# Kernel optimization log

Measured on AMD Instinct MI355X. Metric: run time of the kernel, lower is better.

## Reference

```python
import jax, jax.numpy as jnp
import numpy as np

EPS = 1e-5

def _ln(x, g, b):
    mu = jnp.mean(x, axis=-1, keepdims=True)
    var = jnp.var(x, axis=-1, keepdims=True)
    return (x - mu) * jax.lax.rsqrt(var + EPS) * g + b

def setup_inputs() -> dict:
    key = jax.random.key(0)
    ks = jax.random.split(key, 8)
    B, S, D, DK, DV = 8, 2048, 1024, 128, 128
    sD = 1.0 / np.sqrt(D)
    sDV = 1.0 / np.sqrt(DV)
    sH = 1.0 / np.sqrt(4 * D)
    return {
        "x": jax.random.normal(ks[0], (B, S, D), jnp.float32),
        "ln1_g": jnp.ones((D,), jnp.float32),
        "ln1_b": jnp.zeros((D,), jnp.float32),
        "Wq": jax.random.normal(ks[1], (D, DK), jnp.float32) * sD,
        "bq": jnp.zeros((DK,), jnp.float32),
        "Wk": jax.random.normal(ks[2], (D, DK), jnp.float32) * sD,
        "bk": jnp.zeros((DK,), jnp.float32),
        "Wv": jax.random.normal(ks[3], (D, DV), jnp.float32) * sD,
        "bv": jnp.zeros((DV,), jnp.float32),
        "Wo": jax.random.normal(ks[4], (DV, D), jnp.float32) * sDV,
        "bo": jnp.zeros((D,), jnp.float32),
        "ln2_g": jnp.ones((D,), jnp.float32),
        "ln2_b": jnp.zeros((D,), jnp.float32),
        "W1": jax.random.normal(ks[5], (D, 4 * D), jnp.float32) * sD,
        "b1": jnp.zeros((4 * D,), jnp.float32),
        "W2": jax.random.normal(ks[6], (4 * D, D), jnp.float32) * sH,
        "b2": jnp.zeros((D,), jnp.float32),
    }

def reference(x, ln1_g, ln1_b, Wq, bq, Wk, bk, Wv, bv, Wo, bo, ln2_g, ln2_b, W1, b1, W2, b2):
    # Block.forward (scaling_test=None): pre-LN, naive full attention, residual MLP
    xn = _ln(x, ln1_g, ln1_b)                       # [B,S,D]
    q = xn @ Wq + bq                                # [B,S,DK]
    k = xn @ Wk + bk                                # [B,S,DK]
    v = xn @ Wv + bv                                # [B,S,DV]
    scale = 1.0 / np.sqrt(q.shape[-1])
    S = jnp.einsum("bqd,bkd->bqk", q, k) * scale    # [B,S,S] materialized scores
    A = jax.nn.softmax(S, axis=-1)
    H = jnp.einsum("bqk,bkv->bqv", A, v)            # [B,S,DV]
    y = xn + (H @ Wo + bo)                          # note: residual uses ln1(x), as in source
    h = _ln(y, ln2_g, ln2_b)
    mlp = jax.nn.gelu(h @ W1 + b1, approximate=False) @ W2 + b2
    return y + mlp
```

## Files before the change

kernel.cpp:

```cpp
#include <hip/hip_runtime.h>
#include <math.h>

#define M_TOT   16384
#define D_MODEL 1024
#define D_HEAD  128
#define SEQ     2048
#define NBATCH  8
#define D_FF    4096

typedef _Float16 f16x8 __attribute__((ext_vector_type(8)));
typedef _Float16 f16x4 __attribute__((ext_vector_type(4)));
typedef float    f32x4 __attribute__((ext_vector_type(4)));

#define ATT_SCALE 0.08838834764831845f

__device__ __forceinline__ void gload_lds16(const _Float16* g, _Float16* l) {
  __builtin_amdgcn_global_load_lds(
      (const __attribute__((address_space(1))) unsigned int*)g,
      (__attribute__((address_space(3))) unsigned int*)l, 16, 0, 0);
}
__device__ __forceinline__ unsigned short f16bits(float v) {
  union { _Float16 f; unsigned short u; } cv; cv.f = (_Float16)v; return cv.u;
}
__device__ __forceinline__ float gelu_f(float x) {
  const float t = 0.7978845608028654f * x * (1.0f + 0.044715f * x * x);
  const float e = __expf(2.0f * t);
  const float th = 1.0f - 2.0f / (e + 1.0f);
  return 0.5f * x * (1.0f + th);
}
__device__ __forceinline__ void bar_sync() {
  __asm__ volatile("" ::: "memory");
  __builtin_amdgcn_s_barrier();
  __asm__ volatile("" ::: "memory");
}
__device__ __forceinline__ int swzb(int row, int quad) {
  const int e = (((row & 1) << 2) | quad) ^ ((row >> 1) & 7);
  return ((row >> 1) << 7) | (e << 4);
}
__device__ __forceinline__ void ds_read128o(f16x8& d, unsigned addr, int imm) {
  asm volatile("ds_read_b128 %0, %1 offset:%2" : "=v"(d) : "v"(addr), "i"(imm));
}

__global__ __launch_bounds__(256) void convt_kernel(const float* __restrict__ in,
                                                    _Float16* __restrict__ out,
                                                    int K, int N) {
  __shared__ float t[32][33];
  const int n0 = blockIdx.x * 32, k0 = blockIdx.y * 32;
  const int tx = threadIdx.x & 31, ty = threadIdx.x >> 5;
#pragma unroll
  for (int r = 0; r < 4; r++)
    t[ty + 8 * r][tx] = in[(size_t)(k0 + ty + 8 * r) * N + n0 + tx];
  __syncthreads();
#pragma unroll
  for (int r = 0; r < 4; r++)
    out[(size_t)(n0 + ty + 8 * r) * K + k0 + tx] = (_Float16)t[tx][ty + 8 * r];
}

template <bool WF32>
__global__ __launch_bounds__(256) void ln_kernel(const float* __restrict__ in,
                                                 const float* __restrict__ gamma,
                                                 const float* __restrict__ beta,
                                                 float* __restrict__ of,
                                                 _Float16* __restrict__ oh) {
  __shared__ float shs[4], shq[4];
  const int row = blockIdx.x;
  const int t = threadIdx.x;
  float4 v = ((const float4*)(in + (size_t)row * D_MODEL))[t];
  float s = v.x + v.y + v.z + v.w;
  float q = v.x * v.x + v.y * v.y + v.z * v.z + v.w * v.w;
#pragma unroll
  for (int o = 32; o > 0; o >>= 1) {
    s += __shfl_down(s, o, 64);
    q += __shfl_down(q, o, 64);
  }
  const int lane = t & 63, w = t >> 6;
  if (lane == 0) { shs[w] = s; shq[w] = q; }
  __syncthreads();
  if (t == 0) {
    shs[0] = shs[0] + shs[1] + shs[2] + shs[3];
    shq[0] = shq[0] + shq[1] + shq[2] + shq[3];
  }
  __syncthreads();
  const float mu = shs[0] * (1.0f / D_MODEL);
  const float var = shq[0] * (1.0f / D_MODEL) - mu * mu;
  const float rs = rsqrtf(var + 1e-5f);
  float4 gv = ((const float4*)gamma)[t];
  float4 bv = ((const float4*)beta)[t];
  float4 o;
  o.x = (v.x - mu) * rs * gv.x + bv.x;
  o.y = (v.y - mu) * rs * gv.y + bv.y;
  o.z = (v.z - mu) * rs * gv.z + bv.z;
  o.w = (v.w - mu) * rs * gv.w + bv.w;
  if (WF32) ((float4*)(of + (size_t)row * D_MODEL))[t] = o;
  f16x4 h4 = {(_Float16)o.x, (_Float16)o.y, (_Float16)o.z, (_Float16)o.w};
  ((f16x4*)(oh + (size_t)row * D_MODEL))[t] = h4;
}


struct Frag { f16x8 a[8]; f16x8 b[4]; };

__device__ __forceinline__ void rd_frags(Frag& f, unsigned bA, unsigned bB) {
#pragma unroll
  for (int m = 0; m < 8; ++m) ds_read128o(f.a[m], bA, m * 1024);
#pragma unroll
  for (int n = 0; n < 4; ++n) ds_read128o(f.b[n], bB, n * 1024);
}
__device__ __forceinline__ void mfma32(f32x4 acc[8][4], const Frag& f) {
#pragma unroll
  for (int m = 0; m < 8; ++m)
#pragma unroll
    for (int n = 0; n < 4; ++n)
      acc[m][n] = __builtin_amdgcn_mfma_f32_16x16x32_f16(f.a[m], f.b[n], acc[m][n], 0, 0, 0);
}

#define STAGE_A(JT)                                                       \
  {                                                                       \
    _Float16* ps_ = SM + (((JT) & 3) * 16384) + ldsA;                     \
    const size_t kp_ = (size_t)(JT) * 32;                                 \
    gload_lds16(Ag0 + kp_, ps_);                                          \
    gload_lds16(Ag0 + 16 * (size_t)K + kp_, ps_ + 512);                   \
  }
#define STAGE_B(JT)                                                       \
  {                                                                       \
    _Float16* ps_ = SM + (((JT) & 3) * 16384) + ldsB;                     \
    const size_t kp_ = (size_t)(JT) * 32;                                 \
    gload_lds16(Bg0 + kp_, ps_);                                          \
    gload_lds16(Bg0 + 16 * (size_t)K + kp_, ps_ + 512);                   \
  }

#define KITER(CUR, NXT, JT, RD, PF, WVM)                                       \
  {                                                                            \
    asm volatile("s_waitcnt lgkmcnt(0)" ::: "memory");                         \
    __builtin_amdgcn_sched_barrier(0);                                         \
    bar_sync();                                                                \
    if (RD) {                                                                  \
      const unsigned sb_ = ((unsigned)(((JT) + 1) & 3)) << 15;                 \
      rd_frags(NXT, fbaseA + sb_, fbaseB + sb_);                               \
    }                                                                          \
    if (PF) { STAGE_A((JT) + 3); STAGE_B((JT) + 3); }                          \
    __builtin_amdgcn_sched_barrier(0);                                         \
    __builtin_amdgcn_s_setprio(1);                                             \
    mfma32(acc, CUR);                                                          \
    __builtin_amdgcn_s_setprio(0);                                             \
    if ((WVM) == 4) { asm volatile("s_waitcnt vmcnt(4)" ::: "memory"); bar_sync(); } \
    if ((WVM) == 0) { asm volatile("s_waitcnt vmcnt(0)" ::: "memory"); bar_sync(); } \
  }

template <int MODE>
__global__ __launch_bounds__(512, 2) void mfma_gemm256(
    const _Float16* __restrict__ A, const _Float16* __restrict__ BT,
    const float* __restrict__ bias, const float* __restrict__ res,
    void* __restrict__ Cout, int M, int N, int K) {
  __shared__ __attribute__((aligned(16))) _Float16 SM[4 * 16384];
  const int tid = threadIdx.x;
  const int lane = tid & 63, w = tid >> 6;
  const int l15 = lane & 15, quad = lane >> 4;
  const int wm = w >> 2, wn = w & 3;

  const int nwg = gridDim.x;
  const int bid = (blockIdx.x & 7) * (nwg >> 3) + (blockIdx.x >> 3);
  const int nbx = N >> 8;
  const int bx = bid % nbx, by = bid / nbx;
  const int row0 = by << 8, col0 = bx << 8;

  const int rp = lane >> 3;
  const int el = (lane & 7) ^ rp;
  const int lr = (rp << 1) | (el >> 2);
  const int lc = (el & 3) << 3;
  const _Float16* Ag0 = A + (size_t)(row0 + w * 32 + lr) * K + lc;
  const _Float16* Bg0 = BT + (size_t)(col0 + w * 32 + lr) * K + lc;
  const int ldsA = w * 1024;
  const int ldsB = 8192 + w * 1024;

  const unsigned lds0 =
      (unsigned)(size_t)(__attribute__((address_space(3))) _Float16*)&SM[0];
  const unsigned esw = (unsigned)((((l15 & 1) << 2) | quad) ^ ((l15 >> 1) & 7));
  const unsigned rl128 = (unsigned)(l15 >> 1) << 7;
  const unsigned fbaseA = lds0 + (unsigned)(wm * 8192) + rl128 + (esw << 4);
  const unsigned fbaseB = lds0 + 16384u + (unsigned)(wn * 4096) + rl128 + (esw << 4);

  const f32x4 zero = {0.f, 0.f, 0.f, 0.f};
  f32x4 acc[8][4];
#pragma unroll
  for (int m = 0; m < 8; ++m)
#pragma unroll
    for (int n = 0; n < 4; ++n) acc[m][n] = zero;

  const int NKT = K >> 5;
  Frag fA, fB;

  for (int t = 0; t < 3; ++t) { STAGE_A(t); STAGE_B(t); }
  asm volatile("s_waitcnt vmcnt(4)" ::: "memory");
  bar_sync();
  rd_frags(fA, fbaseA, fbaseB);

  int j = 0;
#pragma unroll 1
  for (; j + 5 < NKT; j += 2) {
    KITER(fA, fB, j,     1, 1, 4);
    KITER(fB, fA, j + 1, 1, 1, 4);
  }
  KITER(fA, fB, NKT - 4, 1, 1, 4);
  KITER(fB, fA, NKT - 3, 1, 0, 0);
  KITER(fA, fB, NKT - 2, 1, 0, -1);
  KITER(fB, fA, NKT - 1, 0, 0, -1);

  const int colb = col0 + wn * 64 + l15;
  if (MODE == 0) {
    float* C = (float*)Cout;
    float bv[4];
#pragma unroll
    for (int n = 0; n < 4; ++n) bv[n] = bias[colb + n * 16];
#pragma unroll
    for (int m = 0; m < 8; ++m)
#pragma unroll
      for (int r = 0; r < 4; ++r) {
        const int row = row0 + wm * 128 + m * 16 + quad * 4 + r;
        const size_t base = (size_t)row * N + colb;
        const float* rp2 = res + base;
        float* cp = C + base;
#pragma unroll
        for (int n = 0; n < 4; ++n) cp[n * 16] = acc[m][n][r] + bv[n] + rp2[n * 16];
      }
  } else {
    _Float16* C = (_Float16*)Cout;
    float bv[4];
#pragma unroll
    for (int n = 0; n < 4; ++n) bv[n] = bias[colb + n * 16];
#pragma unroll
    for (int m = 0; m < 8; ++m)
#pragma unroll
      for (int r = 0; r < 4; ++r) {
        const int row = row0 + wm * 128 + m * 16 + quad * 4 + r;
        _Float16* cp = C + (size_t)row * N + colb;
#pragma unroll
        for (int n = 0; n < 4; ++n) cp[n * 16] = (_Float16)gelu_f(acc[m][n][r] + bv[n]);
      }
  }
  (void)M;
}

template <int MODE>
__global__ __launch_bounds__(256) void mfma_gemm(const _Float16* __restrict__ A,
                                                 const _Float16* __restrict__ BT,
                                                 const float* __restrict__ b0p,
                                                 const float* __restrict__ b1p,
                                                 const float* __restrict__ b2p,
                                                 const float* __restrict__ res,
                                                 void* __restrict__ Cout,
                                                 _Float16* __restrict__ vtout,
                                                 int M, int N, int K) {
  __shared__ _Float16 SMEM[2 * 128 * 32];
  _Float16* As = SMEM;
  _Float16* Bs = SMEM + 128 * 32;
  const int tid = threadIdx.x;
  const int lane = tid & 63, w = tid >> 6;
  const int wr = w >> 1, wc = w & 1;
  const int row0 = blockIdx.y << 7, col0 = blockIdx.x << 7;
  const int l15 = lane & 15, quad = lane >> 4;
  const f32x4 zero = {0.f, 0.f, 0.f, 0.f};
  f32x4 acc[4][4];
#pragma unroll
  for (int i = 0; i < 4; i++)
#pragma unroll
    for (int j = 0; j < 4; j++) acc[i][j] = zero;

  const int srow = lane >> 2;
  const int scol = (lane & 3) << 3;
  const _Float16* Ag = A + (size_t)(row0 + w * 32 + srow) * K + scol;
  const _Float16* Bg = BT + (size_t)(col0 + w * 32 + srow) * K + scol;

  for (int k0 = 0; k0 < K; k0 += 32) {
#pragma unroll
    for (int p = 0; p < 2; p++) {
      gload_lds16(Ag + (size_t)(p * 16) * K + k0, &As[(w * 32 + p * 16) * 32]);
      gload_lds16(Bg + (size_t)(p * 16) * K + k0, &Bs[(w * 32 + p * 16) * 32]);
    }
    __syncthreads();
    f16x8 af[4], bfr[4];
#pragma unroll
    for (int i = 0; i < 4; i++) {
      af[i]  = *(const f16x8*)&As[(wr * 64 + i * 16 + l15) * 32 + quad * 8];
      bfr[i] = *(const f16x8*)&Bs[(wc * 64 + i * 16 + l15) * 32 + quad * 8];
    }
#pragma unroll
    for (int i = 0; i < 4; i++)
#pragma unroll
      for (int j = 0; j < 4; j++)
        acc[i][j] = __builtin_amdgcn_mfma_f32_16x16x32_f16(af[i], bfr[j], acc[i][j], 0, 0, 0);
    __syncthreads();
  }

  if (MODE == 0) {
    float* C = (float*)Cout;
    float bv4[4];
#pragma unroll
    for (int j = 0; j < 4; j++) bv4[j] = b0p[col0 + wc * 64 + j * 16 + l15];
#pragma unroll
    for (int i = 0; i < 4; i++)
#pragma unroll
      for (int r = 0; r < 4; r++) {
        const int row = row0 + wr * 64 + i * 16 + quad * 4 + r;
        const size_t base = (size_t)row * N + col0 + wc * 64 + l15;
        const float* rp = res + base;
        float* cp = C + base;
#pragma unroll
        for (int j = 0; j < 4; j++)
          cp[j * 16] = acc[i][j][r] + bv4[j] + rp[j * 16];
      }
  } else if (MODE == 1) {
    _Float16* C = (_Float16*)Cout;
    float bv4[4];
#pragma unroll
    for (int j = 0; j < 4; j++) bv4[j] = b0p[col0 + wc * 64 + j * 16 + l15];
#pragma unroll
    for (int i = 0; i < 4; i++)
#pragma unroll
      for (int r = 0; r < 4; r++) {
        const int row = row0 + wr * 64 + i * 16 + quad * 4 + r;
        _Float16* cp = C + (size_t)row * N + col0 + wc * 64 + l15;
#pragma unroll
        for (int j = 0; j < 4; j++)
          cp[j * 16] = (_Float16)gelu_f(acc[i][j][r] + bv4[j]);
      }
  } else {
    _Float16* qkout = (_Float16*)Cout;
    const int bx = blockIdx.x;
    if (bx < 2) {
      const float* bp = (bx == 0) ? b0p : b1p;
      const float sc = (bx == 0) ? ATT_SCALE : 1.0f;
      const int cofs = bx * 128 + wc * 64 + l15;
      float bv4[4];
#pragma unroll
      for (int j = 0; j < 4; j++) bv4[j] = bp[wc * 64 + j * 16 + l15];
#pragma unroll
      for (int i = 0; i < 4; i++)
#pragma unroll
        for (int r = 0; r < 4; r++) {
          const int row = row0 + wr * 64 + i * 16 + quad * 4 + r;
          _Float16* cp = qkout + (size_t)row * 256 + cofs;
#pragma unroll
          for (int j = 0; j < 4; j++)
            cp[j * 16] = (_Float16)((acc[i][j][r] + bv4[j]) * sc);
        }
    } else {
      _Float16* Ts = SMEM;
      float bv4[4];
#pragma unroll
      for (int j = 0; j < 4; j++) bv4[j] = b2p[wc * 64 + j * 16 + l15];
      const int bb = row0 >> 11, s0 = row0 & 2047;
#pragma unroll
      for (int c = 0; c < 4; c++) {
        __syncthreads();
        if (wr == (c >> 1)) {
#pragma unroll
          for (int ii = 0; ii < 2; ii++) {
            const int i = (c & 1) * 2 + ii;
#pragma unroll
            for (int j = 0; j < 4; j++) {
              const int vd = wc * 64 + j * 16 + l15;
              const int slocal = ii * 16 + quad * 4;
              ushort4 h;
              h.x = f16bits(acc[i][j][0] + bv4[j]);
              h.y = f16bits(acc[i][j][1] + bv4[j]);
              h.z = f16bits(acc[i][j][2] + bv4[j]);
              h.w = f16bits(acc[i][j][3] + bv4[j]);
              *(ushort4*)&Ts[vd * 40 + slocal] = h;
            }
          }
        }
        __syncthreads();
#pragma unroll
        for (int p = 0; p < 2; p++) {
          const int idx = tid + p * 256;
          const int vd = idx >> 2, s8 = (idx & 3) * 8;
          uint4 d = *(const uint4*)&Ts[vd * 40 + s8];
          *(uint4*)&vtout[((size_t)bb * 128 + vd) * SEQ + s0 + c * 32 + s8] = d;
        }
      }
    }
  }
}

__global__ __launch_bounds__(256) void flash_attn_mfma(const _Float16* __restrict__ qk,
                                                       const _Float16* __restrict__ vt,
                                                       _Float16* __restrict__ H) {
  __shared__ _Float16 Ks[2][64][136];
  __shared__ _Float16 Vs[128][72];
  __shared__ _Float16 Ps[4][16][72];
  const int b = blockIdx.y, q0 = blockIdx.x * 64;
  const int tid = threadIdx.x;
  const int lane = tid & 63, w = tid >> 6;
  const int l15 = lane & 15, quad = lane >> 4;

  f16x8 qf[4];
  {
    const _Float16* qrow = qk + ((size_t)(b * SEQ + q0 + w * 16 + l15)) * 256 + quad * 8;
#pragma unroll
    for (int ks = 0; ks < 4; ks++) qf[ks] = *(const f16x8*)(qrow + ks * 32);
  }
  const f32x4 zero = {0.f, 0.f, 0.f, 0.f};
  f32x4 O[8];
#pragma unroll
  for (int i = 0; i < 8; i++) O[i] = zero;
  float m_r[4] = {-1e30f, -1e30f, -1e30f, -1e30f};
  float l_r[4] = {0.f, 0.f, 0.f, 0.f};

  const _Float16* kg0 = qk + (size_t)(b * SEQ) * 256 + 128 + (size_t)(tid >> 4) * 256 + (tid & 15) * 8;
  const _Float16* vg0 = vt + (size_t)b * 128 * SEQ + (size_t)((tid >> 3)) * SEQ + (tid & 7) * 8;
  uint4 kp[4], vp[4];

#define LOAD_TILE(kt)                                                            \
  {                                                                              \
    const _Float16* kg = kg0 + (size_t)(kt) * 64 * 256;                          \
    const _Float16* vg = vg0 + (size_t)(kt) * 64;                                \
    _Pragma("unroll") for (int p = 0; p < 4; p++) {                              \
      kp[p] = *(const uint4*)(kg + (size_t)p * 16 * 256);                        \
      vp[p] = *(const uint4*)(vg + (size_t)p * 32 * SEQ);                        \
    }                                                                            \
  }
#define STORE_K(buf)                                                             \
  _Pragma("unroll") for (int p = 0; p < 4; p++)                                  \
      *(uint4*)&Ks[buf][(tid >> 4) + 16 * p][(tid & 15) * 8] = kp[p];
#define STORE_V()                                                                \
  _Pragma("unroll") for (int p = 0; p < 4; p++)                                  \
      *(uint4*)&Vs[(tid >> 3) + 32 * p][(tid & 7) * 8] = vp[p];

  LOAD_TILE(0);
  STORE_K(0);
  STORE_V();
  __syncthreads();

  const int NT = SEQ / 64;
  for (int kt = 0; kt < NT; kt++) {
    const int cur = kt & 1;
    if (kt + 1 < NT) LOAD_TILE(kt + 1);

    f32x4 s4[4];
#pragma unroll
    for (int nt = 0; nt < 4; nt++) {
      s4[nt] = zero;
#pragma unroll
      for (int ks = 0; ks < 4; ks++) {
        f16x8 kf = *(const f16x8*)&Ks[cur][nt * 16 + l15][ks * 32 + quad * 8];
        s4[nt] = __builtin_amdgcn_mfma_f32_16x16x32_f16(qf[ks], kf, s4[nt], 0, 0, 0);
      }
    }
    float rmax[4], alpha[4], rsum[4];
#pragma unroll
    for (int r = 0; r < 4; r++)
      rmax[r] = fmaxf(fmaxf(s4[0][r], s4[1][r]), fmaxf(s4[2][r], s4[3][r]));
#pragma unroll
    for (int o = 1; o < 16; o <<= 1)
#pragma unroll
      for (int r = 0; r < 4; r++) rmax[r] = fmaxf(rmax[r], __shfl_xor(rmax[r], o, 64));
#pragma unroll
    for (int r = 0; r < 4; r++) {
      const float nm = fmaxf(m_r[r], rmax[r]);
      alpha[r] = __expf(m_r[r] - nm);
      m_r[r] = nm;
#pragma unroll
      for (int nt = 0; nt < 4; nt++) s4[nt][r] = __expf(s4[nt][r] - nm);
      rsum[r] = s4[0][r] + s4[1][r] + s4[2][r] + s4[3][r];
    }
#pragma unroll
    for (int o = 1; o < 16; o <<= 1)
#pragma unroll
      for (int r = 0; r < 4; r++) rsum[r] += __shfl_xor(rsum[r], o, 64);
#pragma unroll
    for (int r = 0; r < 4; r++) {
      l_r[r] = l_r[r] * alpha[r] + rsum[r];
#pragma unroll
      for (int i = 0; i < 8; i++) O[i][r] *= alpha[r];
    }
#pragma unroll
    for (int nt = 0; nt < 4; nt++)
#pragma unroll
      for (int r = 0; r < 4; r++)
        Ps[w][quad * 4 + r][nt * 16 + l15] = (_Float16)s4[nt][r];
    f16x8 pa[2];
#pragma unroll
    for (int ks = 0; ks < 2; ks++)
      pa[ks] = *(const f16x8*)&Ps[w][l15][ks * 32 + quad * 8];
#pragma unroll
    for (int ks = 0; ks < 2; ks++)
#pragma unroll
      for (int vt8 = 0; vt8 < 8; vt8++) {
        f16x8 vf = *(const f16x8*)&Vs[vt8 * 16 + l15][ks * 32 + quad * 8];
        O[vt8] = __builtin_amdgcn_mfma_f32_16x16x32_f16(pa[ks], vf, O[vt8], 0, 0, 0);
      }

    if (kt + 1 < NT) {
      STORE_K(cur ^ 1);
      __syncthreads();
      STORE_V();
      __syncthreads();
    }
  }
#pragma unroll
  for (int r = 0; r < 4; r++) {
    const float inv = 1.0f / l_r[r];
    _Float16* hp = H + (size_t)(b * SEQ + q0 + w * 16 + quad * 4 + r) * D_HEAD;
#pragma unroll
    for (int vt8 = 0; vt8 < 8; vt8++)
      hp[vt8 * 16 + l15] = (_Float16)(O[vt8][r] * inv);
  }
}

extern "C" void kernel_launch(void* const* d_in, const int* in_sizes, int n_in,
                              void* d_out, int out_size, void* d_ws, size_t ws_size,
                              hipStream_t stream) {
  const float* x     = (const float*)d_in[0];
  const float* ln1_g = (const float*)d_in[1];
  const float* ln1_b = (const float*)d_in[2];
  const float* Wq    = (const float*)d_in[3];
  const float* bq    = (const float*)d_in[4];
  const float* Wk    = (const float*)d_in[5];
  const float* bk    = (const float*)d_in[6];
  const float* Wv    = (const float*)d_in[7];
  const float* bv    = (const float*)d_in[8];
  const float* Wo    = (const float*)d_in[9];
  const float* bo    = (const float*)d_in[10];
  const float* ln2_g = (const float*)d_in[11];
  const float* ln2_b = (const float*)d_in[12];
  const float* W1    = (const float*)d_in[13];
  const float* b1    = (const float*)d_in[14];
  const float* W2    = (const float*)d_in[15];
  const float* b2    = (const float*)d_in[16];
  float* out = (float*)d_out;

  char* ws = (char*)d_ws;
  const size_t MB = 1024 * 1024;
  _Float16* W1T   = (_Float16*)(ws);
  _Float16* W2T   = (_Float16*)(ws + 8 * MB);
  _Float16* WqkvT = (_Float16*)(ws + 16 * MB);
  _Float16* WoT   = (_Float16*)(ws + 16 * MB + 768 * 1024);
  float*    xn_f32 = (float*)(ws + 20 * MB);
  _Float16* xn_f16 = (_Float16*)(ws + 84 * MB);
  _Float16* qkb  = (_Float16*)(ws + 116 * MB);
  _Float16* vtb  = (_Float16*)(ws + 124 * MB);
  _Float16* Hb   = (_Float16*)(ws + 128 * MB);
  _Float16* act  = (_Float16*)(ws + 20 * MB);
  _Float16* h16  = (_Float16*)(ws + 148 * MB);

  convt_kernel<<<dim3(D_FF / 32, D_MODEL / 32), 256, 0, stream>>>(W1, W1T, D_MODEL, D_FF);
  convt_kernel<<<dim3(D_MODEL / 32, D_FF / 32), 256, 0, stream>>>(W2, W2T, D_FF, D_MODEL);
  convt_kernel<<<dim3(D_HEAD / 32, D_MODEL / 32), 256, 0, stream>>>(Wq, WqkvT, D_MODEL, D_HEAD);
  convt_kernel<<<dim3(D_HEAD / 32, D_MODEL / 32), 256, 0, stream>>>(Wk, WqkvT + 128 * 1024, D_MODEL, D_HEAD);
  convt_kernel<<<dim3(D_HEAD / 32, D_MODEL / 32), 256, 0, stream>>>(Wv, WqkvT + 256 * 1024, D_MODEL, D_HEAD);
  convt_kernel<<<dim3(D_MODEL / 32, D_HEAD / 32), 256, 0, stream>>>(Wo, WoT, D_HEAD, D_MODEL);
  ln_kernel<true><<<dim3(M_TOT), 256, 0, stream>>>(x, ln1_g, ln1_b, xn_f32, xn_f16);
  mfma_gemm<2><<<dim3(3, M_TOT / 128), 256, 0, stream>>>(
      xn_f16, WqkvT, bq, bk, bv, nullptr, qkb, vtb, M_TOT, 384, D_MODEL);
  flash_attn_mfma<<<dim3(SEQ / 64, NBATCH), 256, 0, stream>>>(qkb, vtb, Hb);
  mfma_gemm256<0><<<dim3((D_MODEL / 256) * (M_TOT / 256)), 512, 0, stream>>>(
      Hb, WoT, bo, xn_f32, out, M_TOT, D_MODEL, D_HEAD);
  ln_kernel<false><<<dim3(M_TOT), 256, 0, stream>>>(out, ln2_g, ln2_b, nullptr, h16);
  mfma_gemm256<1><<<dim3((D_FF / 256) * (M_TOT / 256)), 512, 0, stream>>>(
      h16, W1T, b1, nullptr, act, M_TOT, D_FF, D_MODEL);
  mfma_gemm256<0><<<dim3((D_MODEL / 256) * (M_TOT / 256)), 512, 0, stream>>>(
      act, W2T, b2, out, out, M_TOT, D_MODEL, D_FF);

  (void)in_sizes; (void)n_in; (void)out_size; (void)ws_size;
}
```

Baseline: 646.5 us.

## Restructure GEMM main loop into four-phase interleaved LDS-read/MFMA/prefetch schedule

Replaces the double-buffered register fragment scheme (read all next-tile fragments while computing the current tile) with a four-phase per-K-tile schedule. Each phase reads a subset of A/B fragments, issues one global-to-LDS prefetch, then runs eight MFMAs, separated by barriers. This cuts register pressure from holding two full fragment sets and spreads global loads across the iteration, but it adds many more barriers per K step and exposes LDS read latency inside each iteration, since there is no cross-iteration fragment prefetch.

```diff
diff --git a/kernel.cpp b/kernel.cpp
--- a/kernel.cpp
+++ b/kernel.cpp
@@ -33,13 +33,10 @@
   __builtin_amdgcn_s_barrier();
   __asm__ volatile("" ::: "memory");
 }
-__device__ __forceinline__ int swzb(int row, int quad) {
-  const int e = (((row & 1) << 2) | quad) ^ ((row >> 1) & 7);
-  return ((row >> 1) << 7) | (e << 4);
-}
 __device__ __forceinline__ void ds_read128o(f16x8& d, unsigned addr, int imm) {
   asm volatile("ds_read_b128 %0, %1 offset:%2" : "=v"(d) : "v"(addr), "i"(imm));
 }
+#define MFMA16(a, b, c) __builtin_amdgcn_mfma_f32_16x16x32_f16((a), (b), (c), 0, 0, 0)
 
 __global__ __launch_bounds__(256) void convt_kernel(const float* __restrict__ in,
                                                     _Float16* __restrict__ out,
@@ -97,51 +94,69 @@
 }
 
 
-struct Frag { f16x8 a[8]; f16x8 b[4]; };
-
-__device__ __forceinline__ void rd_frags(Frag& f, unsigned bA, unsigned bB) {
-#pragma unroll
-  for (int m = 0; m < 8; ++m) ds_read128o(f.a[m], bA, m * 1024);
-#pragma unroll
-  for (int n = 0; n < 4; ++n) ds_read128o(f.b[n], bB, n * 1024);
-}
-__device__ __forceinline__ void mfma32(f32x4 acc[8][4], const Frag& f) {
-#pragma unroll
-  for (int m = 0; m < 8; ++m)
-#pragma unroll
-    for (int n = 0; n < 4; ++n)
-      acc[m][n] = __builtin_amdgcn_mfma_f32_16x16x32_f16(f.a[m], f.b[n], acc[m][n], 0, 0, 0);
-}
-
-#define STAGE_A(JT)                                                       \
-  {                                                                       \
-    _Float16* ps_ = SM + (((JT) & 3) * 16384) + ldsA;                     \
-    const size_t kp_ = (size_t)(JT) * 32;                                 \
-    gload_lds16(Ag0 + kp_, ps_);                                          \
-    gload_lds16(Ag0 + 16 * (size_t)K + kp_, ps_ + 512);                   \
-  }
-#define STAGE_B(JT)                                                       \
-  {                                                                       \
-    _Float16* ps_ = SM + (((JT) & 3) * 16384) + ldsB;                     \
-    const size_t kp_ = (size_t)(JT) * 32;                                 \
-    gload_lds16(Bg0 + kp_, ps_);                                          \
-    gload_lds16(Bg0 + 16 * (size_t)K + kp_, ps_ + 512);                   \
-  }
-
-#define KITER(CUR, NXT, JT, RD, PF, WVM)                                       \
-  {                                                                            \
-    asm volatile("s_waitcnt lgkmcnt(0)" ::: "memory");                         \
-    __builtin_amdgcn_sched_barrier(0);                                         \
-    bar_sync();                                                                \
-    if (RD) {                                                                  \
-      const unsigned sb_ = ((unsigned)(((JT) + 1) & 3)) << 15;                 \
-      rd_frags(NXT, fbaseA + sb_, fbaseB + sb_);                               \
-    }                                                                          \
-    if (PF) { STAGE_A((JT) + 3); STAGE_B((JT) + 3); }                          \
-    __builtin_amdgcn_sched_barrier(0);                                         \
-    __builtin_amdgcn_s_setprio(1);                                             \
-    mfma32(acc, CUR);                                                          \
-    __builtin_amdgcn_s_setprio(0);                                             \
+#define STG_A1(JT) gload_lds16(Ag0 + (size_t)(JT) * 32, SM + (((JT) & 3) * 16384) + ldsA)
+#define STG_A2(JT) gload_lds16(Ag0 + 16 * (size_t)K + (size_t)(JT) * 32, SM + (((JT) & 3) * 16384) + ldsA + 512)
+#define STG_B1(JT) gload_lds16(Bg0 + (size_t)(JT) * 32, SM + (((JT) & 3) * 16384) + ldsB)
+#define STG_B2(JT) gload_lds16(Bg0 + 16 * (size_t)K + (size_t)(JT) * 32, SM + (((JT) & 3) * 16384) + ldsB + 512)
+
+#define KITER4(JT, PF, WVM)                                                         \
+  {                                                                                 \
+    const unsigned sb_ = ((unsigned)((JT) & 3)) << 15;                              \
+    const unsigned bA_ = fbaseA + sb_;                                              \
+    const unsigned bB_ = fbaseB + sb_;                                              \
+    f16x8 fa0, fa1, fa2, fa3, fa4, fa5, fa6, fa7, fb0, fb1, fb2, fb3;               \
+                  \
+    ds_read128o(fa0, bA_, 0);    ds_read128o(fa1, bA_, 1024);                       \
+    ds_read128o(fa2, bA_, 2048); ds_read128o(fa3, bA_, 3072);                       \
+    ds_read128o(fb0, bB_, 0);    ds_read128o(fb1, bB_, 1024);                       \
+    if (PF) { STG_A1((JT) + 3); }                                                   \
+    bar_sync();                                                                     \
+    asm volatile("s_waitcnt lgkmcnt(0)" ::: "memory");                              \
+    __builtin_amdgcn_sched_barrier(0);                                              \
+    __builtin_amdgcn_s_setprio(1);                                                  \
+    acc[0][0] = MFMA16(fa0, fb0, acc[0][0]); acc[0][1] = MFMA16(fa0, fb1, acc[0][1]); \
+    acc[1][0] = MFMA16(fa1, fb0, acc[1][0]); acc[1][1] = MFMA16(fa1, fb1, acc[1][1]); \
+    acc[2][0] = MFMA16(fa2, fb0, acc[2][0]); acc[2][1] = MFMA16(fa2, fb1, acc[2][1]); \
+    acc[3][0] = MFMA16(fa3, fb0, acc[3][0]); acc[3][1] = MFMA16(fa3, fb1, acc[3][1]); \
+    __builtin_amdgcn_s_setprio(0);                                                  \
+    bar_sync();                                                                     \
+                       \
+    ds_read128o(fb2, bB_, 2048); ds_read128o(fb3, bB_, 3072);                       \
+    if (PF) { STG_A2((JT) + 3); }                                                   \
+    bar_sync();                                                                     \
+    asm volatile("s_waitcnt lgkmcnt(0)" ::: "memory");                              \
+    __builtin_amdgcn_sched_barrier(0);                                              \
+    __builtin_amdgcn_s_setprio(1);                                                  \
+    acc[0][2] = MFMA16(fa0, fb2, acc[0][2]); acc[0][3] = MFMA16(fa0, fb3, acc[0][3]); \
+    acc[1][2] = MFMA16(fa1, fb2, acc[1][2]); acc[1][3] = MFMA16(fa1, fb3, acc[1][3]); \
+    acc[2][2] = MFMA16(fa2, fb2, acc[2][2]); acc[2][3] = MFMA16(fa2, fb3, acc[2][3]); \
+    acc[3][2] = MFMA16(fa3, fb2, acc[3][2]); acc[3][3] = MFMA16(fa3, fb3, acc[3][3]); \
+    __builtin_amdgcn_s_setprio(0);                                                  \
+    bar_sync();                                                                     \
+                       \
+    ds_read128o(fa4, bA_, 4096); ds_read128o(fa5, bA_, 5120);                       \
+    ds_read128o(fa6, bA_, 6144); ds_read128o(fa7, bA_, 7168);                       \
+    if (PF) { STG_B1((JT) + 3); }                                                   \
+    bar_sync();                                                                     \
+    asm volatile("s_waitcnt lgkmcnt(0)" ::: "memory");                              \
+    __builtin_amdgcn_sched_barrier(0);                                              \
+    __builtin_amdgcn_s_setprio(1);                                                  \
+    acc[4][0] = MFMA16(fa4, fb0, acc[4][0]); acc[4][1] = MFMA16(fa4, fb1, acc[4][1]); \
+    acc[5][0] = MFMA16(fa5, fb0, acc[5][0]); acc[5][1] = MFMA16(fa5, fb1, acc[5][1]); \
+    acc[6][0] = MFMA16(fa6, fb0, acc[6][0]); acc[6][1] = MFMA16(fa6, fb1, acc[6][1]); \
+    acc[7][0] = MFMA16(fa7, fb0, acc[7][0]); acc[7][1] = MFMA16(fa7, fb1, acc[7][1]); \
+    __builtin_amdgcn_s_setprio(0);                                                  \
+    bar_sync();                                                                     \
+         \
+    if (PF) { STG_B2((JT) + 3); }                                                   \
+    bar_sync();                                                                     \
+    __builtin_amdgcn_s_setprio(1);                                                  \
+    acc[4][2] = MFMA16(fa4, fb2, acc[4][2]); acc[4][3] = MFMA16(fa4, fb3, acc[4][3]); \
+    acc[5][2] = MFMA16(fa5, fb2, acc[5][2]); acc[5][3] = MFMA16(fa5, fb3, acc[5][3]); \
+    acc[6][2] = MFMA16(fa6, fb2, acc[6][2]); acc[6][3] = MFMA16(fa6, fb3, acc[6][3]); \
+    acc[7][2] = MFMA16(fa7, fb2, acc[7][2]); acc[7][3] = MFMA16(fa7, fb3, acc[7][3]); \
+    __builtin_amdgcn_s_setprio(0);                                                  \
+    if ((WVM) == 8) { asm volatile("s_waitcnt vmcnt(8)" ::: "memory"); bar_sync(); } \
     if ((WVM) == 4) { asm volatile("s_waitcnt vmcnt(4)" ::: "memory"); bar_sync(); } \
     if ((WVM) == 0) { asm volatile("s_waitcnt vmcnt(0)" ::: "memory"); bar_sync(); } \
   }
@@ -187,23 +202,17 @@
     for (int n = 0; n < 4; ++n) acc[m][n] = zero;
 
   const int NKT = K >> 5;
-  Frag fA, fB;
-
-  for (int t = 0; t < 3; ++t) { STAGE_A(t); STAGE_B(t); }
-  asm volatile("s_waitcnt vmcnt(4)" ::: "memory");
+
+  for (int t = 0; t < 3; ++t) { STG_A1(t); STG_A2(t); STG_B1(t); STG_B2(t); }
+  asm volatile("s_waitcnt vmcnt(8)" ::: "memory");
   bar_sync();
-  rd_frags(fA, fbaseA, fbaseB);
 
   int j = 0;
 #pragma unroll 1
-  for (; j + 5 < NKT; j += 2) {
-    KITER(fA, fB, j,     1, 1, 4);
-    KITER(fB, fA, j + 1, 1, 1, 4);
-  }
-  KITER(fA, fB, NKT - 4, 1, 1, 4);
-  KITER(fB, fA, NKT - 3, 1, 0, 0);
-  KITER(fA, fB, NKT - 2, 1, 0, -1);
-  KITER(fB, fA, NKT - 1, 0, 0, -1);
+  for (; j + 3 < NKT; ++j) { KITER4(j, 1, 8); }
+  KITER4(NKT - 3, 0, 4);
+  KITER4(NKT - 2, 0, 0);
+  KITER4(NKT - 1, 0, -1);
 
   const int colb = col0 + wn * 64 + l15;
   if (MODE == 0) {
```

Result: no change. 649.7 us (+0.5%).

## Restructure GEMM main loop to 64-wide K tiles with 8-phase interleaved staging

Applied to the files above, without the earlier changes.

Changes the 256x256 f16 MFMA GEMM main loop from 32-wide K tiles with quad buffering to 64-wide K tiles with double buffering. Each K tile is split into four sub-phases, and A/B loads for future tiles are interleaved between MFMA sub-blocks. The LDS layout and swizzle are rewritten to 128-byte rows. The goal is fewer barriers per unit of work and better overlap of global-to-LDS loads with MFMA, at the cost of more barriers per iteration and a more intricate, less flexible schedule.

```diff
diff --git a/kernel.cpp b/kernel.cpp
--- a/kernel.cpp
+++ b/kernel.cpp
@@ -33,13 +33,10 @@
   __builtin_amdgcn_s_barrier();
   __asm__ volatile("" ::: "memory");
 }
-__device__ __forceinline__ int swzb(int row, int quad) {
-  const int e = (((row & 1) << 2) | quad) ^ ((row >> 1) & 7);
-  return ((row >> 1) << 7) | (e << 4);
-}
 __device__ __forceinline__ void ds_read128o(f16x8& d, unsigned addr, int imm) {
   asm volatile("ds_read_b128 %0, %1 offset:%2" : "=v"(d) : "v"(addr), "i"(imm));
 }
+#define MFMA16(a, b, c) __builtin_amdgcn_mfma_f32_16x16x32_f16((a), (b), (c), 0, 0, 0)
 
 __global__ __launch_bounds__(256) void convt_kernel(const float* __restrict__ in,
                                                     _Float16* __restrict__ out,
@@ -97,53 +94,73 @@
 }
 
 
-struct Frag { f16x8 a[8]; f16x8 b[4]; };
-
-__device__ __forceinline__ void rd_frags(Frag& f, unsigned bA, unsigned bB) {
-#pragma unroll
-  for (int m = 0; m < 8; ++m) ds_read128o(f.a[m], bA, m * 1024);
-#pragma unroll
-  for (int n = 0; n < 4; ++n) ds_read128o(f.b[n], bB, n * 1024);
-}
-__device__ __forceinline__ void mfma32(f32x4 acc[8][4], const Frag& f) {
-#pragma unroll
-  for (int m = 0; m < 8; ++m)
-#pragma unroll
-    for (int n = 0; n < 4; ++n)
-      acc[m][n] = __builtin_amdgcn_mfma_f32_16x16x32_f16(f.a[m], f.b[n], acc[m][n], 0, 0, 0);
-}
-
-#define STAGE_A(JT)                                                       \
-  {                                                                       \
-    _Float16* ps_ = SM + (((JT) & 3) * 16384) + ldsA;                     \
-    const size_t kp_ = (size_t)(JT) * 32;                                 \
-    gload_lds16(Ag0 + kp_, ps_);                                          \
-    gload_lds16(Ag0 + 16 * (size_t)K + kp_, ps_ + 512);                   \
-  }
-#define STAGE_B(JT)                                                       \
-  {                                                                       \
-    _Float16* ps_ = SM + (((JT) & 3) * 16384) + ldsB;                     \
-    const size_t kp_ = (size_t)(JT) * 32;                                 \
-    gload_lds16(Bg0 + kp_, ps_);                                          \
-    gload_lds16(Bg0 + 16 * (size_t)K + kp_, ps_ + 512);                   \
-  }
-
-#define KITER(CUR, NXT, JT, RD, PF, WVM)                                       \
-  {                                                                            \
-    asm volatile("s_waitcnt lgkmcnt(0)" ::: "memory");                         \
-    __builtin_amdgcn_sched_barrier(0);                                         \
-    bar_sync();                                                                \
-    if (RD) {                                                                  \
-      const unsigned sb_ = ((unsigned)(((JT) + 1) & 3)) << 15;                 \
-      rd_frags(NXT, fbaseA + sb_, fbaseB + sb_);                               \
-    }                                                                          \
-    if (PF) { STAGE_A((JT) + 3); STAGE_B((JT) + 3); }                          \
-    __builtin_amdgcn_sched_barrier(0);                                         \
-    __builtin_amdgcn_s_setprio(1);                                             \
-    mfma32(acc, CUR);                                                          \
-    __builtin_amdgcn_s_setprio(0);                                             \
-    if ((WVM) == 4) { asm volatile("s_waitcnt vmcnt(4)" ::: "memory"); bar_sync(); } \
-    if ((WVM) == 0) { asm volatile("s_waitcnt vmcnt(0)" ::: "memory"); bar_sync(); } \
+#define STGA(D, H, P, JT)                                                     \
+  gload_lds16(Ag0 + (size_t)((H) * 128 + (P) * 64) * K + (size_t)(JT) * 64,   \
+              SM + (D) * 32768 + (H) * 8192 + (P) * 4096 + wld)
+#define STGB(D, H, P, JT)                                                     \
+  gload_lds16(Bg0 + (size_t)((H) * 128 + (P) * 64) * K + (size_t)(JT) * 64,   \
+              SM + (D) * 32768 + 16384 + (H) * 8192 + (P) * 4096 + wld)
+
+#define RD_A(D, MH)                                                           \
+  _Pragma("unroll") for (int mi = 0; mi < 4; ++mi) {                          \
+    ds_read128o(fa[mi][0], bA[D][0], ((MH) * 4 + mi) * 2048);                 \
+    ds_read128o(fa[mi][1], bA[D][1], ((MH) * 4 + mi) * 2048);                 \
+  }
+#define RD_B(D, NH)                                                           \
+  _Pragma("unroll") for (int ni = 0; ni < 2; ++ni) {                          \
+    ds_read128o(fb[(NH) * 2 + ni][0], bB[D][0], ((NH) * 2 + ni) * 2048);      \
+    ds_read128o(fb[(NH) * 2 + ni][1], bB[D][1], ((NH) * 2 + ni) * 2048);      \
+  }
+#define PH_MFMA(MH, NH)                                                       \
+  bar_sync();                                                                 \
+  asm volatile("s_waitcnt lgkmcnt(0)" ::: "memory");                          \
+  __builtin_amdgcn_sched_barrier(0);                                          \
+  __builtin_amdgcn_s_setprio(1);                                              \
+  _Pragma("unroll") for (int mi = 0; mi < 4; ++mi)                            \
+    _Pragma("unroll") for (int ni = 0; ni < 2; ++ni) {                        \
+      acc[(MH) * 4 + mi][(NH) * 2 + ni] =                                     \
+          MFMA16(fa[mi][0], fb[(NH) * 2 + ni][0], acc[(MH) * 4 + mi][(NH) * 2 + ni]); \
+      acc[(MH) * 4 + mi][(NH) * 2 + ni] =                                     \
+          MFMA16(fa[mi][1], fb[(NH) * 2 + ni][1], acc[(MH) * 4 + mi][(NH) * 2 + ni]); \
+    }                                                                         \
+  __builtin_amdgcn_s_setprio(0);
+
+#define VMW(N)                                                                \
+  if ((N) == 4) { asm volatile("s_waitcnt vmcnt(4)" ::: "memory"); }          \
+  if ((N) == 0) { asm volatile("s_waitcnt vmcnt(0)" ::: "memory"); }
+
+#define ITER8(J, SA1, SB2, SA2, SB3, VM4, VM8)                                \
+  {                                                                           \
+                                                                     \
+    RD_A(0, 0); RD_B(0, 0);                                                   \
+    if (SA1) { STGA(1, 0, 0, (J) + 1); STGA(1, 0, 1, (J) + 1); }              \
+    PH_MFMA(0, 0); bar_sync();                                                \
+                                                                     \
+    RD_B(0, 1);                                                               \
+    if (SA1) { STGA(1, 1, 0, (J) + 1); STGA(1, 1, 1, (J) + 1); }              \
+    PH_MFMA(0, 1); bar_sync();                                                \
+                                                                     \
+    RD_A(0, 1);                                                               \
+    if (SB2) { STGB(0, 0, 0, (J) + 2); STGB(0, 0, 1, (J) + 2); }              \
+    PH_MFMA(1, 0); bar_sync();                                                \
+                                                                     \
+    if (SB2) { STGB(0, 1, 0, (J) + 2); STGB(0, 1, 1, (J) + 2); }              \
+    PH_MFMA(1, 1); VMW(VM4); bar_sync();                                      \
+                                                                     \
+    RD_A(1, 0); RD_B(1, 0);                                                   \
+    if (SA2) { STGA(0, 0, 0, (J) + 2); STGA(0, 0, 1, (J) + 2); }              \
+    PH_MFMA(0, 0); bar_sync();                                                \
+                                                                     \
+    RD_B(1, 1);                                                               \
+    if (SA2) { STGA(0, 1, 0, (J) + 2); STGA(0, 1, 1, (J) + 2); }              \
+    PH_MFMA(0, 1); bar_sync();                                                \
+                                                                     \
+    RD_A(1, 1);                                                               \
+    if (SB3) { STGB(1, 0, 0, (J) + 3); STGB(1, 0, 1, (J) + 3); }              \
+    PH_MFMA(1, 0); bar_sync();                                                \
+                                                                     \
+    if (SB3) { STGB(1, 1, 0, (J) + 3); STGB(1, 1, 1, (J) + 3); }              \
+    PH_MFMA(1, 1); VMW(VM8); bar_sync();                                      \
   }
 
 template <int MODE>
@@ -151,7 +168,7 @@
     const _Float16* __restrict__ A, const _Float16* __restrict__ BT,
     const float* __restrict__ bias, const float* __restrict__ res,
     void* __restrict__ Cout, int M, int N, int K) {
-  __shared__ __attribute__((aligned(16))) _Float16 SM[4 * 16384];
+  __shared__ __attribute__((aligned(16))) _Float16 SM[2 * 32768];
   const int tid = threadIdx.x;
   const int lane = tid & 63, w = tid >> 6;
   const int l15 = lane & 15, quad = lane >> 4;
@@ -163,21 +180,26 @@
   const int bx = bid % nbx, by = bid / nbx;
   const int row0 = by << 8, col0 = bx << 8;
 
-  const int rp = lane >> 3;
-  const int el = (lane & 7) ^ rp;
-  const int lr = (rp << 1) | (el >> 2);
-  const int lc = (el & 3) << 3;
-  const _Float16* Ag0 = A + (size_t)(row0 + w * 32 + lr) * K + lc;
-  const _Float16* Bg0 = BT + (size_t)(col0 + w * 32 + lr) * K + lc;
-  const int ldsA = w * 1024;
-  const int ldsB = 8192 + w * 1024;
+  const int lrS = lane >> 3;
+  const int lcS = ((lane & 7) ^ lrS) * 8;
+  const _Float16* Ag0 = A + (size_t)(row0 + w * 8 + lrS) * K + lcS;
+  const _Float16* Bg0 = BT + (size_t)(col0 + w * 8 + lrS) * K + lcS;
+  const int wld = w * 512;
 
   const unsigned lds0 =
       (unsigned)(size_t)(__attribute__((address_space(3))) _Float16*)&SM[0];
-  const unsigned esw = (unsigned)((((l15 & 1) << 2) | quad) ^ ((l15 >> 1) & 7));
-  const unsigned rl128 = (unsigned)(l15 >> 1) << 7;
-  const unsigned fbaseA = lds0 + (unsigned)(wm * 8192) + rl128 + (esw << 4);
-  const unsigned fbaseB = lds0 + 16384u + (unsigned)(wn * 4096) + rl128 + (esw << 4);
+  const unsigned l7 = (unsigned)(l15 & 7);
+  const unsigned laneRowB = (unsigned)l15 << 7;
+  unsigned bA[2][2], bB[2][2];
+#pragma unroll
+  for (int d = 0; d < 2; ++d)
+#pragma unroll
+    for (int kk = 0; kk < 2; ++kk) {
+      const unsigned ch = (((unsigned)((kk << 2) | quad)) ^ l7) << 4;
+      bA[d][kk] = lds0 + (unsigned)d * 65536u + (unsigned)wm * 16384u + laneRowB + ch;
+      bB[d][kk] = lds0 + (unsigned)d * 65536u + 32768u + (unsigned)(wn >> 1) * 16384u +
+                  (unsigned)(wn & 1) * 8192u + laneRowB + ch;
+    }
 
   const f32x4 zero = {0.f, 0.f, 0.f, 0.f};
   f32x4 acc[8][4];
@@ -185,25 +207,23 @@
   for (int m = 0; m < 8; ++m)
 #pragma unroll
     for (int n = 0; n < 4; ++n) acc[m][n] = zero;
-
-  const int NKT = K >> 5;
-  Frag fA, fB;
-
-  for (int t = 0; t < 3; ++t) { STAGE_A(t); STAGE_B(t); }
+  f16x8 fa[4][2], fb[4][2];
+
+  const int NKT = K >> 6;
+  const int niter = NKT >> 1;
+
+#pragma unroll
+  for (int h = 0; h < 2; ++h) { STGA(0, h, 0, 0); STGA(0, h, 1, 0); }
+#pragma unroll
+  for (int h = 0; h < 2; ++h) { STGB(0, h, 0, 0); STGB(0, h, 1, 0); }
+#pragma unroll
+  for (int h = 0; h < 2; ++h) { STGB(1, h, 0, 1); STGB(1, h, 1, 1); }
   asm volatile("s_waitcnt vmcnt(4)" ::: "memory");
   bar_sync();
-  rd_frags(fA, fbaseA, fbaseB);
-
-  int j = 0;
+
 #pragma unroll 1
-  for (; j + 5 < NKT; j += 2) {
-    KITER(fA, fB, j,     1, 1, 4);
-    KITER(fB, fA, j + 1, 1, 1, 4);
-  }
-  KITER(fA, fB, NKT - 4, 1, 1, 4);
-  KITER(fB, fA, NKT - 3, 1, 0, 0);
-  KITER(fA, fB, NKT - 2, 1, 0, -1);
-  KITER(fB, fA, NKT - 1, 0, 0, -1);
+  for (int i = 0; i + 1 < niter; ++i) { ITER8(2 * i, 1, 1, 1, 1, 4, 4); }
+  ITER8(NKT - 2, 1, 0, 0, 0, 0, -1);
 
   const int colb = col0 + wn * 64 + l15;
   if (MODE == 0) {
```

New measurement: 638.4 us. No clear change (-1.3%).
